# Optimization experiments

Measured on AMD Instinct MI355X. Metric: run time of the kernel, lower is better.

## Reference

```python
import jax, jax.numpy as jnp
import numpy as np

B, S, H = 32, 2048, 1024

def setup_inputs() -> dict:
    key = jax.random.key(0)
    k1, k2, k3, k4, k5 = jax.random.split(key, 5)
    return {
        "hidden": jax.random.normal(k1, (B, H), dtype=jnp.float32),
        "encoder_outputs": jax.random.normal(k2, (B, S, H), dtype=jnp.float32),
        "W_attn": jax.random.normal(k3, (H, H), dtype=jnp.float32) * (1.0 / np.sqrt(H)),
        "b_attn": jax.random.normal(k4, (H,), dtype=jnp.float32) * 0.01,
        "v": jax.random.uniform(k5, (H,), dtype=jnp.float32),
    }

def reference(hidden, encoder_outputs, W_attn, b_attn, v):
    # energy = tanh((enc + hidden[:,None,:]) @ W^T + b)  -> [B,S,H]
    x = encoder_outputs + hidden[:, None, :]
    energy = jnp.tanh(jnp.einsum('bsh,oh->bso', x, W_attn) + b_attn)
    scores = jnp.einsum('bsh,h->bs', energy, v)            # [B,S]
    attn_weights = jax.nn.softmax(scores, axis=1)          # [B,S]
    context = jnp.einsum('bs,bsh->bh', attn_weights, encoder_outputs)  # [B,H]
    return (context, attn_weights)
```

## Files before the change

### kernel.cpp

```cpp
#include <hip/hip_runtime.h>
#include <hip/hip_bf16.h>

#define BATCH 32
#define SEQ   2048
#define HID   1024
#define M_TOT (BATCH*SEQ)
#define NG    32

typedef __attribute__((ext_vector_type(8))) short          bf16x8;
typedef __attribute__((ext_vector_type(8))) unsigned short us8;
typedef __attribute__((ext_vector_type(4))) float          f32x4;
typedef __attribute__((ext_vector_type(4))) unsigned       u32x4;

__device__ __forceinline__ unsigned short f2bf_rn(float x) {
    unsigned u = __float_as_uint(x);
    return (unsigned short)((u + 0x7fffu + ((u >> 16) & 1u)) >> 16);
}
__device__ __forceinline__ float bf2f(unsigned short h) {
    return __uint_as_float(((unsigned)h) << 16);
}
__device__ __forceinline__ unsigned cvt_pk_bf16(float s0, float s1) {
    unsigned r;
    asm("v_cvt_pk_bf16_f32 %0, %1, %2" : "=v"(r) : "v"(s0), "v"(s1));
    return r;
}

using as1_cv = const __attribute__((address_space(1))) void;
using as3_v  = __attribute__((address_space(3))) void;
__device__ __forceinline__ void gload16(const void* g, char* s) {
    __builtin_amdgcn_global_load_lds((as1_cv*)g, (as3_v*)s, 16, 0, 0);
}

#define FENCE() asm volatile("" ::: "memory")

__global__ __launch_bounds__(256) void k_convW(const float* __restrict__ W,
                                               unsigned short* __restrict__ w2) {
    const int i8 = (blockIdx.x * 256 + threadIdx.x) * 8;
    const int o = i8 >> 10, h = i8 & 1023;
    float4 w0 = *(const float4*)(W + i8);
    float4 w1 = *(const float4*)(W + i8 + 4);
    float xs[8] = {w0.x, w0.y, w0.z, w0.w, w1.x, w1.y, w1.z, w1.w};
    us8 hv{}, lv{};
#pragma unroll
    for (int t = 0; t < 8; t++) {
        unsigned short xh = f2bf_rn(xs[t]);
        hv[t] = (unsigned short)xh;
        lv[t] = (unsigned short)f2bf_rn(xs[t] - bf2f(xh));
    }
    *(us8*)(w2 + (size_t)o * 2048 + h)        = hv;
    *(us8*)(w2 + (size_t)o * 2048 + 1024 + h) = lv;
}

__global__ __launch_bounds__(512, 2) void k_gemm_scores(
    const float* __restrict__ enc,
    const float* __restrict__ hidden,
    const unsigned short* __restrict__ w2,
    const float* __restrict__ b_attn,
    const float* __restrict__ v,
    float* __restrict__ pscore8)
{
    extern __shared__ char smem[];
    float* hidL = (float*)(smem + 65536);

    const int tid  = threadIdx.x;
    const int lane = tid & 63, wid = tid >> 6;
    const int wr = wid >> 1, wc = wid & 1;
    const int fr = lane & 15, g = lane >> 4;
    const int gsw = (g ^ ((fr >> 1) & 3)) * 16;

    const int bid  = blockIdx.x;
    const int swz  = (bid & 7) * 128 + (bid >> 3);
    const int mbase = (swz >> 2) * 256;
    const int nbase = (swz & 3) * 256;
    const int bidx  = mbase >> 11;

    const float* encBase = enc + (size_t)(mbase + wr * 64 + fr) * HID + g * 8;

    const int brow  = wid * 16 + (lane >> 2);
    const int bsx8  = ((lane & 3) ^ ((lane >> 3) & 3)) * 8;

    *(float2*)(hidL + tid * 2) = *(const float2*)(hidden + (size_t)bidx * HID + tid * 2);

    f32x4 acc[4][8];
#pragma unroll
    for (int i = 0; i < 4; i++)
#pragma unroll
        for (int j = 0; j < 8; j++) acc[i][j] = (f32x4)0.f;

    bf16x8 FH[4], FL[4];
    float4 er[8];

    auto loadEncAll = [&](int Gn) {
#pragma unroll
        for (int s = 0; s < 4; s++) {
            const float* ep = encBase + (size_t)(s * 16) * HID + Gn * 32;
            er[s * 2]     = *(const float4*)ep;
            er[s * 2 + 1] = *(const float4*)(ep + 4);
        }
    };
    auto convAll = [&](const float* hv) {
#pragma unroll
        for (int s = 0; s < 4; s++) {
            float4 e0 = er[s * 2], e1 = er[s * 2 + 1];
            float x0 = e0.x + hv[0], x1 = e0.y + hv[1];
            float x2 = e0.z + hv[2], x3 = e0.w + hv[3];
            float x4 = e1.x + hv[4], x5 = e1.y + hv[5];
            float x6 = e1.z + hv[6], x7 = e1.w + hv[7];
            unsigned h01 = cvt_pk_bf16(x0, x1);
            unsigned h23 = cvt_pk_bf16(x2, x3);
            unsigned h45 = cvt_pk_bf16(x4, x5);
            unsigned h67 = cvt_pk_bf16(x6, x7);
            unsigned l01 = cvt_pk_bf16(x0 - __uint_as_float(h01 << 16),
                                       x1 - __uint_as_float(h01 & 0xffff0000u));
            unsigned l23 = cvt_pk_bf16(x2 - __uint_as_float(h23 << 16),
                                       x3 - __uint_as_float(h23 & 0xffff0000u));
            unsigned l45 = cvt_pk_bf16(x4 - __uint_as_float(h45 << 16),
                                       x5 - __uint_as_float(h45 & 0xffff0000u));
            unsigned l67 = cvt_pk_bf16(x6 - __uint_as_float(h67 << 16),
                                       x7 - __uint_as_float(h67 & 0xffff0000u));
            union { u32x4 u; bf16x8 b; } H, L;
            H.u[0] = h01; H.u[1] = h23; H.u[2] = h45; H.u[3] = h67;
            L.u[0] = l01; L.u[1] = l23; L.u[2] = l45; L.u[3] = l67;
            FH[s] = H.b;
            FL[s] = L.b;
        }
    };
    auto stageB = [&](int G2, int part) {
        const unsigned short* s0 = w2 + (size_t)(nbase + brow) * 2048 + part * 1024 + G2 * 32 + bsx8;
        char* d0 = smem + (G2 & 1) * 32768 + part * 16384 + wid * 1024;
        gload16(s0, d0);
        gload16(s0 + (size_t)128 * 2048, d0 + 8192);
    };
    auto rdB = [&](int slot, int part, int j) -> bf16x8 {
        return *(const bf16x8*)(smem + slot * 32768 + part * 16384 +
                                (wc * 128 + j * 16 + fr) * 64 + gsw);
    };

    stageB(0, 0); stageB(0, 1);
    loadEncAll(0);
    asm volatile("s_waitcnt lgkmcnt(0)" ::: "memory");
    __builtin_amdgcn_s_barrier(); FENCE();
    {
        float hv[8];
        *(float4*)&hv[0] = *(const float4*)(hidL + g * 8);
        *(float4*)&hv[4] = *(const float4*)(hidL + g * 8 + 4);
        convAll(hv);
    }

    for (int G = 0; G < NG; ++G) {
        const int slot = G & 1;
        asm volatile("s_waitcnt vmcnt(0)" ::: "memory");
        __builtin_amdgcn_s_barrier(); FENCE();

        if (G + 1 < NG) {
            stageB(G + 1, 0); stageB(G + 1, 1);
            loadEncAll(G + 1);
        }

        bf16x8 bh[8];
#pragma unroll
        for (int j = 0; j < 8; j++) bh[j] = rdB(slot, 0, j);

        __builtin_amdgcn_s_setprio(1);
#pragma unroll
        for (int j = 0; j < 8; j++)
#pragma unroll
            for (int i = 0; i < 4; i++)
                acc[i][j] = __builtin_amdgcn_mfma_f32_16x16x32_bf16(FH[i], bh[j], acc[i][j], 0, 0, 0);
#pragma unroll
        for (int j = 0; j < 8; j++)
#pragma unroll
            for (int i = 0; i < 4; i++)
                acc[i][j] = __builtin_amdgcn_mfma_f32_16x16x32_bf16(FL[i], bh[j], acc[i][j], 0, 0, 0);
        __builtin_amdgcn_s_setprio(0);
#pragma unroll
        for (int j = 0; j < 8; j++) {
            bf16x8 blj = rdB(slot, 1, j);
            __builtin_amdgcn_s_setprio(1);
#pragma unroll
            for (int i = 0; i < 4; i++)
                acc[i][j] = __builtin_amdgcn_mfma_f32_16x16x32_bf16(FH[i], blj, acc[i][j], 0, 0, 0);
            __builtin_amdgcn_s_setprio(0);
        }

        if (G + 1 < NG) {
            float hv[8];
            *(float4*)&hv[0] = *(const float4*)(hidL + (G + 1) * 32 + g * 8);
            *(float4*)&hv[4] = *(const float4*)(hidL + (G + 1) * 32 + g * 8 + 4);
            convAll(hv);
        }
    }

    float rs[4][4];
#pragma unroll
    for (int i = 0; i < 4; i++)
#pragma unroll
        for (int r = 0; r < 4; r++) rs[i][r] = 0.f;

#pragma unroll
    for (int j = 0; j < 8; j++) {
        const int n = nbase + wc * 128 + j * 16 + fr;
        const float ba = b_attn[n];
        const float vv = v[n];
#pragma unroll
        for (int i = 0; i < 4; i++)
#pragma unroll
            for (int r = 0; r < 4; r++) {
                float e  = acc[i][j][r] + ba;
                float ex = __expf(2.f * e);
                rs[i][r] += (1.f - 2.f / (ex + 1.f)) * vv;
            }
    }
#pragma unroll
    for (int off = 1; off < 16; off <<= 1)
#pragma unroll
        for (int i = 0; i < 4; i++)
#pragma unroll
            for (int r = 0; r < 4; r++) rs[i][r] += __shfl_xor(rs[i][r], off, 64);

    float v0 = 0.f;
#pragma unroll
    for (int i = 0; i < 4; i++)
#pragma unroll
        for (int r = 0; r < 4; r++)
            if (fr == i * 4 + r) v0 = rs[i][r];

    const int plane = (swz & 3) * 2 + wc;
    pscore8[(size_t)plane * M_TOT + mbase + wr * 64 +
            (fr >> 2) * 16 + g * 4 + (fr & 3)] = v0;
}

__global__ __launch_bounds__(256) void k_softmax(const float* __restrict__ ps,
                                                 float* __restrict__ out) {
    const int b = blockIdx.x, t = threadIdx.x;
    __shared__ float red[8];
    float loc[8];
    float lmax = -1e30f;
#pragma unroll
    for (int i = 0; i < 8; i++) {
        const int s = t + i * 256;
        float sc = 0.f;
#pragma unroll
        for (int p = 0; p < 8; p++) sc += ps[(size_t)p * M_TOT + (size_t)b * SEQ + s];
        loc[i] = sc;
        lmax = fmaxf(lmax, sc);
    }
    for (int o = 32; o; o >>= 1) lmax = fmaxf(lmax, __shfl_xor(lmax, o, 64));
    if ((t & 63) == 0) red[t >> 6] = lmax;
    __syncthreads();
    const float bmax = fmaxf(fmaxf(red[0], red[1]), fmaxf(red[2], red[3]));
    float ev[8], lsum = 0.f;
#pragma unroll
    for (int i = 0; i < 8; i++) { ev[i] = expf(loc[i] - bmax); lsum += ev[i]; }
    for (int o = 32; o; o >>= 1) lsum += __shfl_xor(lsum, o, 64);
    __syncthreads();
    if ((t & 63) == 0) red[4 + (t >> 6)] = lsum;
    __syncthreads();
    const float inv = 1.f / (red[4] + red[5] + red[6] + red[7]);
#pragma unroll
    for (int i = 0; i < 8; i++)
        out[(size_t)BATCH * HID + (size_t)b * SEQ + t + i * 256] = ev[i] * inv;
}

__global__ __launch_bounds__(256) void k_pctx(const float* __restrict__ enc,
                                              const float* __restrict__ attn,
                                              float* __restrict__ pctx) {
    const int hc = blockIdx.x, scb = blockIdx.y, b = blockIdx.z;
    const int h = hc * 256 + threadIdx.x;
    const float* ap = attn + (size_t)b * SEQ + scb * 256;
    const float* ep = enc + ((size_t)b * SEQ + scb * 256) * HID + h;
    float a = 0.f;
#pragma unroll 4
    for (int s = 0; s < 256; s++) a += ap[s] * ep[(size_t)s * HID];
    pctx[((size_t)scb * BATCH + b) * HID + h] = a;
}

__global__ __launch_bounds__(256) void k_ctx(const float* __restrict__ pctx,
                                             float* __restrict__ out) {
    const int i = blockIdx.x * 256 + threadIdx.x;
    float a = 0.f;
#pragma unroll
    for (int p = 0; p < 8; p++) a += pctx[(size_t)p * BATCH * HID + i];
    out[i] = a;
}

extern "C" void kernel_launch(void* const* d_in, const int* in_sizes, int n_in,
                              void* d_out, int out_size, void* d_ws, size_t ws_size,
                              hipStream_t stream) {
    const float* hidden = (const float*)d_in[0];
    const float* enc    = (const float*)d_in[1];
    const float* W      = (const float*)d_in[2];
    const float* b_attn = (const float*)d_in[3];
    const float* v      = (const float*)d_in[4];
    float* out = (float*)d_out;

    char* ws = (char*)d_ws;
    unsigned short* w2 = (unsigned short*)ws;
    float* pscore8     = (float*)(ws + ((size_t)4 << 20));
    float* pctx        = (float*)ws;

    const int smemBytes = 65536 + 4096;
    hipFuncSetAttribute((const void*)k_gemm_scores,
                        hipFuncAttributeMaxDynamicSharedMemorySize, smemBytes);

    k_convW<<<dim3(512), dim3(256), 0, stream>>>(W, w2);
    k_gemm_scores<<<dim3(1024), dim3(512), smemBytes, stream>>>(
        enc, hidden, w2, b_attn, v, pscore8);
    k_softmax<<<dim3(BATCH), dim3(256), 0, stream>>>(pscore8, out);
    k_pctx<<<dim3(4, 8, BATCH), dim3(256), 0, stream>>>(enc, out + BATCH * HID, pctx);
    k_ctx<<<dim3(128), dim3(256), 0, stream>>>(pctx, out);
}
```

Before: 449.2 us.

## Precompute hidden@W^T+b per batch and interleave conversion with MFMAs

Uses linearity to move the hidden-state term out of the main GEMM: a small kernel computes hidden@W^T + b per batch, and the scores kernel adds it as a per-batch bias instead of adding hidden to every encoder element before bf16 splitting. This removes the LDS hidden buffer, its barrier and the per-element adds, and shrinks shared memory. The third MFMA pass is restructured to load all B fragments up front and interleave the next encoder conversion with MFMAs using sched_group_barrier hints. It adds an extra launch and changes rounding slightly, since enc rather than enc+hidden is now split into bf16 hi/lo.

```diff
diff --git a/kernel.cpp b/kernel.cpp
--- a/kernel.cpp
+++ b/kernel.cpp
@@ -51,16 +51,35 @@
     *(us8*)(w2 + (size_t)o * 2048 + 1024 + h) = lv;
 }
 
+__global__ __launch_bounds__(256) void k_hw(const float* __restrict__ W,
+                                            const float* __restrict__ hidden,
+                                            const float* __restrict__ b_attn,
+                                            float* __restrict__ cb) {
+    __shared__ float hid[HID];
+    const int t = threadIdx.x, b = blockIdx.y;
+#pragma unroll
+    for (int i = 0; i < 4; i++)
+        hid[t + i * 256] = hidden[(size_t)b * HID + t + i * 256];
+    __syncthreads();
+    const int n = blockIdx.x * 256 + t;
+    const float* wr = W + (size_t)n * HID;
+    float a = 0.f;
+#pragma unroll 4
+    for (int k = 0; k < HID; k += 4) {
+        float4 w4 = *(const float4*)(wr + k);
+        a += w4.x * hid[k] + w4.y * hid[k + 1] + w4.z * hid[k + 2] + w4.w * hid[k + 3];
+    }
+    cb[(size_t)b * HID + n] = a + b_attn[n];
+}
+
 __global__ __launch_bounds__(512, 2) void k_gemm_scores(
     const float* __restrict__ enc,
-    const float* __restrict__ hidden,
     const unsigned short* __restrict__ w2,
-    const float* __restrict__ b_attn,
+    const float* __restrict__ cb,
     const float* __restrict__ v,
     float* __restrict__ pscore8)
 {
     extern __shared__ char smem[];
-    float* hidL = (float*)(smem + 65536);
 
     const int tid  = threadIdx.x;
     const int lane = tid & 63, wid = tid >> 6;
@@ -78,8 +97,6 @@
 
     const int brow  = wid * 16 + (lane >> 2);
     const int bsx8  = ((lane & 3) ^ ((lane >> 3) & 3)) * 8;
-
-    *(float2*)(hidL + tid * 2) = *(const float2*)(hidden + (size_t)bidx * HID + tid * 2);
 
     f32x4 acc[4][8];
 #pragma unroll
@@ -98,32 +115,25 @@
             er[s * 2 + 1] = *(const float4*)(ep + 4);
         }
     };
-    auto convAll = [&](const float* hv) {
-#pragma unroll
-        for (int s = 0; s < 4; s++) {
-            float4 e0 = er[s * 2], e1 = er[s * 2 + 1];
-            float x0 = e0.x + hv[0], x1 = e0.y + hv[1];
-            float x2 = e0.z + hv[2], x3 = e0.w + hv[3];
-            float x4 = e1.x + hv[4], x5 = e1.y + hv[5];
-            float x6 = e1.z + hv[6], x7 = e1.w + hv[7];
-            unsigned h01 = cvt_pk_bf16(x0, x1);
-            unsigned h23 = cvt_pk_bf16(x2, x3);
-            unsigned h45 = cvt_pk_bf16(x4, x5);
-            unsigned h67 = cvt_pk_bf16(x6, x7);
-            unsigned l01 = cvt_pk_bf16(x0 - __uint_as_float(h01 << 16),
-                                       x1 - __uint_as_float(h01 & 0xffff0000u));
-            unsigned l23 = cvt_pk_bf16(x2 - __uint_as_float(h23 << 16),
-                                       x3 - __uint_as_float(h23 & 0xffff0000u));
-            unsigned l45 = cvt_pk_bf16(x4 - __uint_as_float(h45 << 16),
-                                       x5 - __uint_as_float(h45 & 0xffff0000u));
-            unsigned l67 = cvt_pk_bf16(x6 - __uint_as_float(h67 << 16),
-                                       x7 - __uint_as_float(h67 & 0xffff0000u));
-            union { u32x4 u; bf16x8 b; } H, L;
-            H.u[0] = h01; H.u[1] = h23; H.u[2] = h45; H.u[3] = h67;
-            L.u[0] = l01; L.u[1] = l23; L.u[2] = l45; L.u[3] = l67;
-            FH[s] = H.b;
-            FL[s] = L.b;
-        }
+    auto convSet = [&](int s) {
+        float4 e0 = er[s * 2], e1 = er[s * 2 + 1];
+        unsigned h01 = cvt_pk_bf16(e0.x, e0.y);
+        unsigned h23 = cvt_pk_bf16(e0.z, e0.w);
+        unsigned h45 = cvt_pk_bf16(e1.x, e1.y);
+        unsigned h67 = cvt_pk_bf16(e1.z, e1.w);
+        unsigned l01 = cvt_pk_bf16(e0.x - __uint_as_float(h01 << 16),
+                                   e0.y - __uint_as_float(h01 & 0xffff0000u));
+        unsigned l23 = cvt_pk_bf16(e0.z - __uint_as_float(h23 << 16),
+                                   e0.w - __uint_as_float(h23 & 0xffff0000u));
+        unsigned l45 = cvt_pk_bf16(e1.x - __uint_as_float(h45 << 16),
+                                   e1.y - __uint_as_float(h45 & 0xffff0000u));
+        unsigned l67 = cvt_pk_bf16(e1.z - __uint_as_float(h67 << 16),
+                                   e1.w - __uint_as_float(h67 & 0xffff0000u));
+        union { u32x4 u; bf16x8 b; } H, L;
+        H.u[0] = h01; H.u[1] = h23; H.u[2] = h45; H.u[3] = h67;
+        L.u[0] = l01; L.u[1] = l23; L.u[2] = l45; L.u[3] = l67;
+        FH[s] = H.b;
+        FL[s] = L.b;
     };
     auto stageB = [&](int G2, int part) {
         const unsigned short* s0 = w2 + (size_t)(nbase + brow) * 2048 + part * 1024 + G2 * 32 + bsx8;
@@ -138,14 +148,8 @@
 
     stageB(0, 0); stageB(0, 1);
     loadEncAll(0);
-    asm volatile("s_waitcnt lgkmcnt(0)" ::: "memory");
-    __builtin_amdgcn_s_barrier(); FENCE();
-    {
-        float hv[8];
-        *(float4*)&hv[0] = *(const float4*)(hidL + g * 8);
-        *(float4*)&hv[4] = *(const float4*)(hidL + g * 8 + 4);
-        convAll(hv);
-    }
+#pragma unroll
+    for (int s = 0; s < 4; s++) convSet(s);
 
     for (int G = 0; G < NG; ++G) {
         const int slot = G & 1;
@@ -173,21 +177,21 @@
             for (int i = 0; i < 4; i++)
                 acc[i][j] = __builtin_amdgcn_mfma_f32_16x16x32_bf16(FL[i], bh[j], acc[i][j], 0, 0, 0);
         __builtin_amdgcn_s_setprio(0);
-#pragma unroll
-        for (int j = 0; j < 8; j++) {
-            bf16x8 blj = rdB(slot, 1, j);
+
+        bf16x8 bl[8];
+#pragma unroll
+        for (int j = 0; j < 8; j++) bl[j] = rdB(slot, 1, j);
+
+#pragma unroll
+        for (int i = 0; i < 4; i++) {
             __builtin_amdgcn_s_setprio(1);
 #pragma unroll
-            for (int i = 0; i < 4; i++)
-                acc[i][j] = __builtin_amdgcn_mfma_f32_16x16x32_bf16(FH[i], blj, acc[i][j], 0, 0, 0);
+            for (int j = 0; j < 8; j++)
+                acc[i][j] = __builtin_amdgcn_mfma_f32_16x16x32_bf16(FH[i], bl[j], acc[i][j], 0, 0, 0);
             __builtin_amdgcn_s_setprio(0);
-        }
-
-        if (G + 1 < NG) {
-            float hv[8];
-            *(float4*)&hv[0] = *(const float4*)(hidL + (G + 1) * 32 + g * 8);
-            *(float4*)&hv[4] = *(const float4*)(hidL + (G + 1) * 32 + g * 8 + 4);
-            convAll(hv);
+            if (G + 1 < NG) convSet(i);
+            __builtin_amdgcn_sched_group_barrier(0x008, 8, 0);
+            __builtin_amdgcn_sched_group_barrier(0x002, 28, 0);
         }
     }
 
@@ -200,7 +204,7 @@
 #pragma unroll
     for (int j = 0; j < 8; j++) {
         const int n = nbase + wc * 128 + j * 16 + fr;
-        const float ba = b_attn[n];
+        const float ba = cb[(size_t)bidx * HID + n];
         const float vv = v[n];
 #pragma unroll
         for (int i = 0; i < 4; i++)
@@ -297,15 +301,17 @@
     char* ws = (char*)d_ws;
     unsigned short* w2 = (unsigned short*)ws;
     float* pscore8     = (float*)(ws + ((size_t)4 << 20));
+    float* cb          = (float*)(ws + ((size_t)6 << 20));
     float* pctx        = (float*)ws;
 
-    const int smemBytes = 65536 + 4096;
+    const int smemBytes = 65536;
     hipFuncSetAttribute((const void*)k_gemm_scores,
                         hipFuncAttributeMaxDynamicSharedMemorySize, smemBytes);
 
     k_convW<<<dim3(512), dim3(256), 0, stream>>>(W, w2);
+    k_hw<<<dim3(4, 32), dim3(256), 0, stream>>>(W, hidden, b_attn, cb);
     k_gemm_scores<<<dim3(1024), dim3(512), smemBytes, stream>>>(
-        enc, hidden, w2, b_attn, v, pscore8);
+        enc, w2, cb, v, pscore8);
     k_softmax<<<dim3(BATCH), dim3(256), 0, stream>>>(pscore8, out);
     k_pctx<<<dim3(4, 8, BATCH), dim3(256), 0, stream>>>(enc, out + BATCH * HID, pctx);
     k_ctx<<<dim3(128), dim3(256), 0, stream>>>(pctx, out);
```

Result: slower. 487.3 us (+8.5%).
